# Kernel tuning notes

Measured on AMD Instinct MI355X. Metric: run time of the kernel, lower is better.

The kernel has to match this reference:

```python
import jax, jax.numpy as jnp
import numpy as np
import math

B, S, HID = 2, 2048, 1024
NH = 16
HD = HID // NH          # 64
VD = HD // 2            # 32 value dim
TD = HD - VD            # 32 type dim
EPS = 1e-6


def setup_inputs() -> dict:
    key = jax.random.key(0)
    ks = jax.random.split(key, 12)
    std = 1.0 / math.sqrt(HID)
    xav = math.sqrt(6.0 / (TD + TD))
    return {
        "x": jax.random.normal(ks[0], (B, S, HID), dtype=jnp.float32),
        "q_w": jax.random.uniform(ks[1], (HID, HID), jnp.float32, -std, std),
        "q_b": jax.random.uniform(ks[2], (HID,), jnp.float32, -std, std),
        "k_w": jax.random.uniform(ks[3], (HID, HID), jnp.float32, -std, std),
        "k_b": jax.random.uniform(ks[4], (HID,), jnp.float32, -std, std),
        "v_w": jax.random.uniform(ks[5], (HID, HID), jnp.float32, -std, std),
        "v_b": jax.random.uniform(ks[6], (HID,), jnp.float32, -std, std),
        "out_w": jax.random.uniform(ks[7], (HID, HID), jnp.float32, -std, std),
        "out_b": jax.random.uniform(ks[8], (HID,), jnp.float32, -std, std),
        "type_bilinear": jax.random.uniform(ks[9], (NH, TD, TD), jnp.float32, -xav, xav),
        "type_bias": jnp.full((NH,), 2.0, dtype=jnp.float32),
        "mask": jnp.ones((B, S), dtype=jnp.int32),
    }


def reference(x, q_w, q_b, k_w, k_b, v_w, v_b, out_w, out_b, type_bilinear, type_bias, mask):
    # projections: [B,S,HID] -> [B,NH,S,HD]
    def proj(w, b):
        y = jnp.einsum("bsi,io->bso", x, w) + b
        return y.reshape(B, S, NH, HD).transpose(0, 2, 1, 3)

    q = proj(q_w, q_b)
    k = proj(k_w, k_b)
    v = proj(v_w, v_b)

    q_val, q_type = q[..., :VD], q[..., VD:]
    k_val, k_type = k[..., :VD], k[..., VD:]

    # standard value score: [B,NH,S,S]
    val_scores = jnp.einsum("bhqd,bhkd->bhqk", q_val, k_val) / math.sqrt(VD)

    # per-head bilinear type score: q_type @ W_h @ k_type^T + bias_h
    qt = jnp.einsum("bhqd,hde->bhqe", q_type, type_bilinear)
    type_scores = jnp.einsum("bhqe,bhke->bhqk", qt, k_type) + type_bias[None, :, None, None]
    type_unif = jax.nn.sigmoid(type_scores)

    scores = val_scores + jnp.log(type_unif + EPS)

    # mask: [B,S] -> broadcast over heads and query dim (keys masked)
    m = (mask[:, None, None, :] != 0)
    scores = jnp.where(m, scores, -jnp.inf)

    attn = jax.nn.softmax(scores, axis=-1)
    out = jnp.einsum("bhqk,bhkd->bhqd", attn, v)          # [B,NH,S,HD]
    out = out.transpose(0, 2, 1, 3).reshape(B, S, HID)
    return jnp.einsum("bsi,io->bso", out, out_w) + out_b
```

## Files before the change

### kernel.cpp

```cpp
#include <hip/hip_runtime.h>
#include <hip/hip_bf16.h>
#include <math.h>

typedef __attribute__((ext_vector_type(8))) short bf16x8;
typedef __attribute__((ext_vector_type(4))) short bf16x4;
typedef __attribute__((ext_vector_type(4))) float f32x4;
typedef __attribute__((ext_vector_type(4))) int   i32x4;

#define NHh 16
#define Sq  2048
#define HIDq 1024
#define HDq 64
#define LOG2E 1.4426950408889634f

#if __has_builtin(__builtin_amdgcn_exp2f)
#define EXP2F(x) __builtin_amdgcn_exp2f(x)
#else
#define EXP2F(x) exp2f(x)
#endif
#if __has_builtin(__builtin_amdgcn_rcpf)
#define RCPF(x) __builtin_amdgcn_rcpf(x)
#else
#define RCPF(x) (1.0f/(x))
#endif

#if __has_builtin(__builtin_amdgcn_mfma_f32_16x16x16bf16_1k)
__device__ __forceinline__ f32x4 MFMA16(bf16x4 a, bf16x4 b, f32x4 c){
  return __builtin_amdgcn_mfma_f32_16x16x16bf16_1k(a, b, c, 0, 0, 0);
}
#else
__device__ __forceinline__ f32x4 MFMA16(bf16x4 a, bf16x4 b, f32x4 c){
  asm volatile("v_mfma_f32_16x16x16_bf16 %0, %1, %2, %0\n\ts_nop 7\n\ts_nop 7"
               : "+v"(c) : "v"(a), "v"(b));
  return c;
}
#endif

__device__ __forceinline__ unsigned short f2bf(float f){
  union { float f; unsigned u; } v; v.f = f;
  unsigned r = v.u + 0x7fffu + ((v.u >> 16) & 1u);
  return (unsigned short)(r >> 16);
}
__device__ __forceinline__ float bf2f(unsigned short s){
  union { unsigned u; float f; } v; v.u = ((unsigned)s) << 16;
  return v.f;
}
__device__ __forceinline__ unsigned pk2bf(float lo, float hi){
  union { __hip_bfloat162 h; unsigned u; } w;
  w.h = __float22bfloat162_rn(make_float2(lo, hi));
  return w.u;
}

__device__ __forceinline__ void gload_lds16(const unsigned short* g, unsigned short* l){
  __builtin_amdgcn_global_load_lds(
      (const __attribute__((address_space(1))) unsigned int*)g,
      (__attribute__((address_space(3))) unsigned int*)l, 16, 0, 0);
}

__global__ __launch_bounds__(256) void convert_x(const float* __restrict__ in,
                                                 unsigned short* __restrict__ out, int n8,
                                                 const int* __restrict__ mask,
                                                 unsigned short* __restrict__ Mbf){
  int bid = blockIdx.x;
  int nmain = gridDim.x - 2;
  if (bid >= nmain){
    int base = (bid - nmain)*2048 + threadIdx.x*8;
    #pragma unroll
    for (int j=0;j<8;j++) Mbf[base+j] = mask[base+j] ? (unsigned short)0x3F80 : (unsigned short)0;
    return;
  }
  int i = bid*256 + threadIdx.x;
  if (i >= n8) return;
  const f32x4* p = (const f32x4*)(in + (size_t)i*8);
  f32x4 a = p[0], b = p[1];
  union { unsigned short us[8]; i32x4 v; } o;
  #pragma unroll
  for (int j=0;j<4;j++){ o.us[j] = f2bf(a[j]); o.us[4+j] = f2bf(b[j]); }
  *(i32x4*)(out + (size_t)i*8) = o.v;
}

__global__ __launch_bounds__(256) void transpose_w(const float* __restrict__ w0, const float* __restrict__ w1,
                                                   const float* __restrict__ w2, const float* __restrict__ w3,
                                                   unsigned short* __restrict__ wT){
  __shared__ float tile[32][33];
  int z = blockIdx.z;
  const float* w = (z==0)?w0:(z==1)?w1:(z==2)?w2:w3;
  unsigned short* dst = wT + (size_t)z*HIDq*HIDq;
  int tx = threadIdx.x, ty = threadIdx.y;
  int n0 = blockIdx.x*32, k0 = blockIdx.y*32;
  #pragma unroll
  for (int i=ty;i<32;i+=8) tile[i][tx] = w[(size_t)(k0+i)*HIDq + n0+tx];
  __syncthreads();
  #pragma unroll
  for (int i=ty;i<32;i+=8) dst[(size_t)(n0+i)*HIDq + k0+tx] = f2bf(tile[tx][i]);
}

__device__ __forceinline__ void gemm_core_gl(const unsigned short* __restrict__ Ag,
                                             const unsigned short* __restrict__ Bg,
                                             unsigned short* As, unsigned short* Bs,
                                             int t, int wv, int lane, int wr, int wc, int lr, int g,
                                             f32x4 acc[4][4]){
  for (int k0=0; k0<HIDq; k0+=64){
    __syncthreads();
    #pragma unroll
    for (int j=0;j<4;j++){
      int flat = (j*4+wv)*64 + lane;
      int row = flat>>3, c = flat&7;
      int srcc = (c ^ (row&7))*8;
      gload_lds16(Ag + (size_t)row*HIDq + k0 + srcc, &As[flat*8]);
      gload_lds16(Bg + (size_t)row*HIDq + k0 + srcc, &Bs[flat*8]);
    }
    __syncthreads();
    #pragma unroll
    for (int ks=0; ks<2; ks++){
      bf16x8 af[4], bfv[4];
      #pragma unroll
      for (int m=0;m<4;m++){
        int rr = wr + m*16 + lr;
        af[m]  = *(bf16x8*)&As[rr*64 + (((ks*4+g) ^ (rr&7))*8)];
      }
      #pragma unroll
      for (int n=0;n<4;n++){
        int rr = wc + n*16 + lr;
        bfv[n] = *(bf16x8*)&Bs[rr*64 + (((ks*4+g) ^ (rr&7))*8)];
      }
      #pragma unroll
      for (int n=0;n<4;n++)
        #pragma unroll
        for (int m=0;m<4;m++)
          acc[n][m] = __builtin_amdgcn_mfma_f32_16x16x32_bf16(bfv[n], af[m], acc[n][m], 0,0,0);
    }
  }
}

__global__ __launch_bounds__(256) void gemm_qkv(const unsigned short* __restrict__ xbf,
    const unsigned short* __restrict__ wT,
    const float* __restrict__ q_b, const float* __restrict__ k_b, const float* __restrict__ v_b,
    const int* __restrict__ mask,
    unsigned short* __restrict__ Qeff, unsigned short* __restrict__ Keff,
    unsigned short* __restrict__ Vt){
  __shared__ unsigned short As[128*64];
  __shared__ unsigned short Bs[128*64];
  const int t = threadIdx.x;
  const int wv = t>>6, lane = t&63, g = lane>>4, lr = lane&15;
  const int wr = (wv>>1)*64, wc = (wv&1)*64;
  f32x4 acc[4][4] = {};
  const int xb = blockIdx.x, yb = blockIdx.y;
  const float VS = 0.25501335f;

  if (xb < 16){
    const int row0 = yb*128, col0 = xb*128;
    gemm_core_gl(xbf + (size_t)row0*HIDq, wT + (size_t)col0*HIDq, As, Bs, t, wv, lane, wr, wc, lr, g, acc);
    #pragma unroll
    for (int n=0;n<4;n++){
      #pragma unroll
      for (int m=0;m<4;m++){
        int row = row0 + wr + m*16 + lr;
        int b_ = row>>11, ss = row&2047;
        int colb = col0 + wc + n*16 + g*4;
        int seg = colb>>10, cw = colb&1023;
        int hh = cw>>6, d = cw&63;
        const float* bp = seg ? k_b : q_b;
        f32x4 bb = *(const f32x4*)&bp[cw];
        float sc = seg ? 1.0f : (d < 32 ? VS : -LOG2E);
        unsigned short* E = seg ? Keff : Qeff;
        float v0 = (acc[n][m][0]+bb[0])*sc, v1 = (acc[n][m][1]+bb[1])*sc;
        float v2 = (acc[n][m][2]+bb[2])*sc, v3 = (acc[n][m][3]+bb[3])*sc;
        union { unsigned u[2]; unsigned long long ll; } W;
        W.u[0] = pk2bf(v0,v1); W.u[1] = pk2bf(v2,v3);
        *(unsigned long long*)&E[(((size_t)b_*NHh+hh)*Sq+ss)*HDq + d] = W.ll;
      }
    }
  } else {
    const int row0 = (xb-16)*128, col0 = yb*128;
    gemm_core_gl(wT + (size_t)2*HIDq*HIDq + (size_t)row0*HIDq, xbf + (size_t)col0*HIDq,
                 As, Bs, t, wv, lane, wr, wc, lr, g, acc);
    #pragma unroll
    for (int n=0;n<4;n++){
      #pragma unroll
      for (int m=0;m<4;m++){
        int chan = row0 + wr + m*16 + lr;
        int hh = chan>>6, d = chan&63;
        float bv = v_b[chan];
        int colb = col0 + wc + n*16 + g*4;
        int b_ = colb>>11, ss = colb&2047;
        i32x4 mk = *(const i32x4*)&mask[(size_t)b_*Sq + ss];
        float m0 = mk[0]?1.f:0.f, m1 = mk[1]?1.f:0.f, m2 = mk[2]?1.f:0.f, m3 = mk[3]?1.f:0.f;
        union { unsigned u[2]; unsigned long long ll; } W;
        W.u[0] = pk2bf((acc[n][m][0]+bv)*m0, (acc[n][m][1]+bv)*m1);
        W.u[1] = pk2bf((acc[n][m][2]+bv)*m2, (acc[n][m][3]+bv)*m3);
        *(unsigned long long*)&Vt[(((size_t)b_*NHh+hh)*HDq + d)*Sq + ss] = W.ll;
      }
    }
  }
}

__global__ __launch_bounds__(256) void gemm_out(const unsigned short* __restrict__ A,
                                                const unsigned short* __restrict__ Bt,
                                                const float* __restrict__ bias,
                                                float* __restrict__ C){
  __shared__ unsigned short As[128*64];
  __shared__ unsigned short Bs[64*64];
  const int t = threadIdx.x;
  const int wv = t>>6, lane = t&63, g = lane>>4, lr = lane&15;
  const int wr = (wv>>1)*64, wc = (wv&1)*32;
  const int row0 = blockIdx.y*128, col0 = blockIdx.x*64;
  f32x4 acc[2][4] = {};
  for (int k0=0; k0<HIDq; k0+=64){
    __syncthreads();
    #pragma unroll
    for (int j=0;j<4;j++){
      int flat = t + j*256;
      int row = flat>>3, c = flat&7;
      int srcc = (c ^ (row&7))*8;
      gload_lds16(A + (size_t)(row0+row)*HIDq + k0 + srcc, &As[flat*8]);
    }
    #pragma unroll
    for (int j=0;j<2;j++){
      int flat = t + j*256;
      int row = flat>>3, c = flat&7;
      int srcc = (c ^ (row&7))*8;
      gload_lds16(Bt + (size_t)(col0+row)*HIDq + k0 + srcc, &Bs[flat*8]);
    }
    __syncthreads();
    #pragma unroll
    for (int ks=0; ks<2; ks++){
      bf16x8 af[4], bfv[2];
      #pragma unroll
      for (int m=0;m<4;m++){
        int rr = wr + m*16 + lr;
        af[m]  = *(bf16x8*)&As[rr*64 + (((ks*4+g) ^ (rr&7))*8)];
      }
      #pragma unroll
      for (int n=0;n<2;n++){
        int rr = wc + n*16 + lr;
        bfv[n] = *(bf16x8*)&Bs[rr*64 + (((ks*4+g) ^ (rr&7))*8)];
      }
      #pragma unroll
      for (int n=0;n<2;n++)
        #pragma unroll
        for (int m=0;m<4;m++)
          acc[n][m] = __builtin_amdgcn_mfma_f32_16x16x32_bf16(bfv[n], af[m], acc[n][m], 0,0,0);
    }
  }
  #pragma unroll
  for (int n=0;n<2;n++){
    #pragma unroll
    for (int m=0;m<4;m++){
      int row = row0 + wr + m*16 + lr;
      int colb = col0 + wc + n*16 + g*4;
      f32x4 bb = *(const f32x4*)&bias[colb];
      f32x4 o = acc[n][m] + bb;
      *(f32x4*)&C[(size_t)row*HIDq + colb] = o;
    }
  }
}

__global__ __launch_bounds__(256,2) void attn_kernel(
    const unsigned short* __restrict__ Qe, const unsigned short* __restrict__ Ke,
    const unsigned short* __restrict__ Vt, const float* __restrict__ Tb,
    const float* __restrict__ tbias, const unsigned short* __restrict__ Mbf,
    unsigned short* __restrict__ Obuf)
{
  __shared__ __align__(16) unsigned char smem[36864];
  unsigned short* Kb0 = (unsigned short*)smem;
  unsigned short* Kb1 = (unsigned short*)(smem + 8192);
  unsigned short* Vb0 = (unsigned short*)(smem + 16384);
  unsigned short* Vb1 = (unsigned short*)(smem + 24576);
  unsigned short* Msk = (unsigned short*)(smem + 32768);
  float* qls = (float*)smem;
  unsigned short* qtls = (unsigned short*)(smem + 24576);

  const int t = threadIdx.x;
  const int dd = blockIdx.x;
  const int slot = dd>>3, xcd = dd&7;
  const int x = slot & 15;
  const int bh = ((slot>>4)<<3) | xcd;
  const int h = bh & 15, b = bh >> 4;
  const int q0 = x*128;
  const int wv = t>>6, lane = t&63, g = lane>>4, lr = lane&15;

  const unsigned short* Qb  = Qe + (((size_t)b*NHh+h)*Sq + q0)*HDq;
  const unsigned short* Kb  = Ke + ((size_t)b*NHh+h)*(size_t)Sq*HDq;
  const unsigned short* Vtb = Vt + ((size_t)b*NHh+h)*(size_t)HDq*Sq;
  const unsigned short* Mbfb = Mbf + (size_t)b*Sq;

  {
    int row = t>>1, c8 = (t&1)*16;
    bf16x8 v0 = *(const bf16x8*)(Qb + (size_t)row*HDq + 32 + c8);
    bf16x8 v1 = *(const bf16x8*)(Qb + (size_t)row*HDq + 32 + c8 + 8);
    #pragma unroll
    for (int j=0;j<8;j++){
      qls[row*33 + c8 + j]     = bf2f((unsigned short)v0[j]);
      qls[row*33 + c8 + 8 + j] = bf2f((unsigned short)v1[j]);
    }
  }
  __syncthreads();
  {
    const float* Th = Tb + (size_t)h*1024;
    #pragma unroll
    for (int rp=0; rp<2; rp++){
      int row = rp*64 + (t&63), e0 = (t>>6)*8;
      float a[8] = {};
      #pragma unroll 4
      for (int d=0; d<32; d++){
        float qd = qls[row*33 + d];
        const f32x4* tp = (const f32x4*)(Th + d*32 + e0);
        f32x4 t0 = tp[0], t1 = tp[1];
        a[0]+=qd*t0[0]; a[1]+=qd*t0[1]; a[2]+=qd*t0[2]; a[3]+=qd*t0[3];
        a[4]+=qd*t1[0]; a[5]+=qd*t1[1]; a[6]+=qd*t1[2]; a[7]+=qd*t1[3];
      }
      union { unsigned u[2]; unsigned long long ll; } W0, W1;
      W0.u[0]=pk2bf(a[0],a[1]); W0.u[1]=pk2bf(a[2],a[3]);
      W1.u[0]=pk2bf(a[4],a[5]); W1.u[1]=pk2bf(a[6],a[7]);
      *(unsigned long long*)&qtls[row*40 + e0]     = W0.ll;
      *(unsigned long long*)&qtls[row*40 + e0 + 4] = W1.ll;
    }
  }
  bf16x8 qvf0 = *(const bf16x8*)(Qb + (size_t)(wv*32+lr)*HDq + g*8);
  bf16x8 qvf1 = *(const bf16x8*)(Qb + (size_t)(wv*32+16+lr)*HDq + g*8);
  __syncthreads();
  bf16x8 qtn0 = *(const bf16x8*)&qtls[(wv*32+lr)*40 + g*8];
  bf16x8 qtn1 = *(const bf16x8*)&qtls[(wv*32+16+lr)*40 + g*8];
  __syncthreads();

  gload_lds16(Mbfb + t*8, Msk + t*8);
  #pragma unroll
  for (int i=0;i<2;i++){
    int c = t + i*256;
    int kr = c>>3, kc = c&7;
    gload_lds16(Kb + (size_t)kr*HDq + ((kc ^ (kr&7))*8), Kb0 + c*8);
    int vd = c>>3, vc = c&7;
    gload_lds16(Vtb + (size_t)vd*Sq + ((vc ^ (vd&7))*8), Vb0 + c*8);
  }
  __syncthreads();

  const float tbn = -tbias[h]*LOG2E;
  const f32x4 tbc = {tbn,tbn,tbn,tbn};
  const f32x4 zf = {0.f,0.f,0.f,0.f};
  f32x4 oT0[4] = {}, oT1[4] = {};
  f32x4 lsum0 = {0.f,0.f,0.f,0.f}, lsum1 = {0.f,0.f,0.f,0.f};

  auto phase = [&](const unsigned short* Kc, const unsigned short* Vc, int key0,
                   bool doStage, int keyN, unsigned short* Kn, unsigned short* Vn){
    if (doStage){
      #pragma unroll
      for (int i=0;i<2;i++){
        int c = t + i*256;
        int kr = c>>3, kc = c&7;
        gload_lds16(Kb + (size_t)(keyN+kr)*HDq + ((kc ^ (kr&7))*8), Kn + c*8);
        int vd = c>>3, vc = c&7;
        gload_lds16(Vtb + (size_t)vd*Sq + keyN + ((vc ^ (vd&7))*8), Vn + c*8);
      }
      asm volatile("s_waitcnt vmcnt(4)" ::: "memory");
    } else {
      asm volatile("s_waitcnt vmcnt(0)" ::: "memory");
    }
    __builtin_amdgcn_sched_barrier(0);
    __builtin_amdgcn_s_barrier();

    f32x4 sv0[4], st0[4], sv1[4], st1[4];
    __builtin_amdgcn_s_setprio(1);
    #pragma unroll
    for (int ks=0; ks<4; ks++){
      const unsigned short* kb = Kc + (ks*16+lr)*64;
      bf16x8 kf0 = *(const bf16x8*)(kb + (((g  ) ^ (lr&7))*8));
      bf16x8 kf1 = *(const bf16x8*)(kb + (((4+g) ^ (lr&7))*8));
      sv0[ks] = __builtin_amdgcn_mfma_f32_16x16x32_bf16(kf0, qvf0, zf, 0,0,0);
      st0[ks] = __builtin_amdgcn_mfma_f32_16x16x32_bf16(kf1, qtn0, tbc, 0,0,0);
      sv1[ks] = __builtin_amdgcn_mfma_f32_16x16x32_bf16(kf0, qvf1, zf, 0,0,0);
      st1[ks] = __builtin_amdgcn_mfma_f32_16x16x32_bf16(kf1, qtn1, tbc, 0,0,0);
    }
    __builtin_amdgcn_s_setprio(0);
    bf16x4 pa0[4], pa1[4];
    #pragma unroll
    for (int ks=0; ks<4; ks++){
      {
        float p0 = EXP2F(sv0[ks][0]) * RCPF(1.f + EXP2F(st0[ks][0]));
        float p1 = EXP2F(sv0[ks][1]) * RCPF(1.f + EXP2F(st0[ks][1]));
        float p2 = EXP2F(sv0[ks][2]) * RCPF(1.f + EXP2F(st0[ks][2]));
        float p3 = EXP2F(sv0[ks][3]) * RCPF(1.f + EXP2F(st0[ks][3]));
        union { unsigned u[2]; bf16x4 v; } P_;
        P_.u[0] = pk2bf(p0,p1); P_.u[1] = pk2bf(p2,p3);
        pa0[ks] = P_.v;
      }
      {
        float p0 = EXP2F(sv1[ks][0]) * RCPF(1.f + EXP2F(st1[ks][0]));
        float p1 = EXP2F(sv1[ks][1]) * RCPF(1.f + EXP2F(st1[ks][1]));
        float p2 = EXP2F(sv1[ks][2]) * RCPF(1.f + EXP2F(st1[ks][2]));
        float p3 = EXP2F(sv1[ks][3]) * RCPF(1.f + EXP2F(st1[ks][3]));
        union { unsigned u[2]; bf16x4 v; } P_;
        P_.u[0] = pk2bf(p0,p1); P_.u[1] = pk2bf(p2,p3);
        pa1[ks] = P_.v;
      }
    }
    #pragma unroll
    for (int ks=0; ks<4; ks++){
      bf16x4 mfr = *(const bf16x4*)(Msk + key0 + ks*16 + g*4);
      __builtin_amdgcn_s_setprio(1);
      lsum0 = MFMA16(pa0[ks], mfr, lsum0);
      lsum1 = MFMA16(pa1[ks], mfr, lsum1);
      #pragma unroll
      for (int db=0; db<4; db++){
        bf16x4 vf = *(const bf16x4*)(Vc + (db*16+lr)*64 + (((2*ks + (g>>1)) ^ (lr&7))*8 + 4*(g&1)));
        oT0[db] = MFMA16(pa0[ks], vf, oT0[db]);
        oT1[db] = MFMA16(pa1[ks], vf, oT1[db]);
      }
      __builtin_amdgcn_s_setprio(0);
    }
    __builtin_amdgcn_s_barrier();
  };

  for (int kt=0; kt<Sq; kt+=128){
    phase(Kb0, Vb0, kt,      true,           kt+64,  Kb1, Vb1);
    phase(Kb1, Vb1, kt+64,   kt+128 < Sq,    kt+128, Kb0, Vb0);
  }

  float linv0[4], linv1[4];
  #pragma unroll
  for (int r=0;r<4;r++){
    linv0[r] = (lsum0[r] > 0.f) ? RCPF(lsum0[r]) : 0.f;
    linv1[r] = (lsum1[r] > 0.f) ? RCPF(lsum1[r]) : 0.f;
  }
  {
    unsigned short* Ob = Obuf + ((size_t)b*Sq + (q0 + wv*32 + g*4))*HIDq + h*HDq + lr;
    #pragma unroll
    for (int db=0; db<4; db++)
      #pragma unroll
      for (int r=0;r<4;r++)
        Ob[(size_t)r*HIDq + db*16] = f2bf(oT0[db][r]*linv0[r]);
  }
  {
    unsigned short* Ob = Obuf + ((size_t)b*Sq + (q0 + wv*32 + 16 + g*4))*HIDq + h*HDq + lr;
    #pragma unroll
    for (int db=0; db<4; db++)
      #pragma unroll
      for (int r=0;r<4;r++)
        Ob[(size_t)r*HIDq + db*16] = f2bf(oT1[db][r]*linv1[r]);
  }
}

extern "C" void kernel_launch(void* const* d_in, const int* in_sizes, int n_in,
                              void* d_out, int out_size, void* d_ws, size_t ws_size,
                              hipStream_t stream) {
  const float* x     = (const float*)d_in[0];
  const float* q_w   = (const float*)d_in[1];
  const float* q_b   = (const float*)d_in[2];
  const float* k_w   = (const float*)d_in[3];
  const float* k_b   = (const float*)d_in[4];
  const float* v_w   = (const float*)d_in[5];
  const float* v_b   = (const float*)d_in[6];
  const float* out_w = (const float*)d_in[7];
  const float* out_b = (const float*)d_in[8];
  const float* Tb    = (const float*)d_in[9];
  const float* tbias = (const float*)d_in[10];
  const int*   mask  = (const int*)d_in[11];

  const size_t MROWS = 4096;
  unsigned short* xbf  = (unsigned short*)d_ws;
  unsigned short* wT   = xbf  + MROWS*HIDq;
  unsigned short* Qeff = wT   + (size_t)4*HIDq*HIDq;
  unsigned short* Keff = Qeff + MROWS*HIDq;
  unsigned short* Vt   = Keff + MROWS*HIDq;
  unsigned short* Obuf = Vt   + MROWS*HIDq;
  unsigned short* Mbf  = Obuf + MROWS*HIDq;

  int n8 = (int)(MROWS*HIDq/8);
  convert_x<<<dim3(n8/256 + 2), dim3(256), 0, stream>>>(x, xbf, n8, mask, Mbf);
  transpose_w<<<dim3(32,32,4), dim3(32,8), 0, stream>>>(q_w, k_w, v_w, out_w, wT);

  gemm_qkv<<<dim3(24,32), dim3(256), 0, stream>>>(xbf, wT, q_b, k_b, v_b, mask, Qeff, Keff, Vt);

  attn_kernel<<<dim3(512), dim3(256), 0, stream>>>(Qeff, Keff, Vt, Tb, tbias, Mbf, Obuf);

  gemm_out<<<dim3(16,32), dim3(256), 0, stream>>>(Obuf, wT + (size_t)3*HIDq*HIDq, out_b, (float*)d_out);
}
```

Baseline: 154.3 us.

## Split attention over key halves, fold type bilinear into Q weights

The attention kernel now splits the key range into two halves, doubling the grid to 1024 blocks with a higher occupancy target. Each half writes a normalized partial output and its row sums, and a new merge kernel combines them. The per-block type-bilinear transform of Q is removed; a fold_T kernel multiplies the Q weights and bias by the bilinear matrix once per call, so the QKV GEMM emits the transformed Q directly. The convert and transpose prep kernels are fused into one launch, and gemm_qkv blocks are remapped across XCDs. The cost is an extra merge pass, partial results stored in bf16, and buffer reuse of the xbf and wT regions for partials.

```diff
diff --git a/kernel.cpp b/kernel.cpp
--- a/kernel.cpp
+++ b/kernel.cpp
@@ -57,42 +57,80 @@
       (__attribute__((address_space(3))) unsigned int*)l, 16, 0, 0);
 }
 
-__global__ __launch_bounds__(256) void convert_x(const float* __restrict__ in,
-                                                 unsigned short* __restrict__ out, int n8,
-                                                 const int* __restrict__ mask,
-                                                 unsigned short* __restrict__ Mbf){
+__global__ __launch_bounds__(256) void prep(const float* __restrict__ x,
+                                            unsigned short* __restrict__ xbf,
+                                            const int* __restrict__ mask,
+                                            unsigned short* __restrict__ Mbf,
+                                            const float* __restrict__ w0, const float* __restrict__ w1,
+                                            const float* __restrict__ w2, const float* __restrict__ w3,
+                                            unsigned short* __restrict__ wT){
   int bid = blockIdx.x;
-  int nmain = gridDim.x - 2;
-  if (bid >= nmain){
-    int base = (bid - nmain)*2048 + threadIdx.x*8;
+  int t = threadIdx.x;
+  if (bid < 2048){
+    int i = bid*256 + t;
+    const f32x4* p = (const f32x4*)(x + (size_t)i*8);
+    f32x4 a = p[0], b = p[1];
+    union { unsigned short us[8]; i32x4 v; } o;
+    #pragma unroll
+    for (int j=0;j<4;j++){ o.us[j] = f2bf(a[j]); o.us[4+j] = f2bf(b[j]); }
+    *(i32x4*)(xbf + (size_t)i*8) = o.v;
+  } else if (bid < 2050){
+    int base = (bid - 2048)*2048 + t*8;
     #pragma unroll
     for (int j=0;j<8;j++) Mbf[base+j] = mask[base+j] ? (unsigned short)0x3F80 : (unsigned short)0;
-    return;
-  }
-  int i = bid*256 + threadIdx.x;
-  if (i >= n8) return;
-  const f32x4* p = (const f32x4*)(in + (size_t)i*8);
-  f32x4 a = p[0], b = p[1];
-  union { unsigned short us[8]; i32x4 v; } o;
-  #pragma unroll
-  for (int j=0;j<4;j++){ o.us[j] = f2bf(a[j]); o.us[4+j] = f2bf(b[j]); }
-  *(i32x4*)(out + (size_t)i*8) = o.v;
-}
-
-__global__ __launch_bounds__(256) void transpose_w(const float* __restrict__ w0, const float* __restrict__ w1,
-                                                   const float* __restrict__ w2, const float* __restrict__ w3,
-                                                   unsigned short* __restrict__ wT){
-  __shared__ float tile[32][33];
-  int z = blockIdx.z;
-  const float* w = (z==0)?w0:(z==1)?w1:(z==2)?w2:w3;
-  unsigned short* dst = wT + (size_t)z*HIDq*HIDq;
-  int tx = threadIdx.x, ty = threadIdx.y;
-  int n0 = blockIdx.x*32, k0 = blockIdx.y*32;
-  #pragma unroll
-  for (int i=ty;i<32;i+=8) tile[i][tx] = w[(size_t)(k0+i)*HIDq + n0+tx];
+  } else {
+    __shared__ float tile[32][33];
+    int bid2 = bid - 2050;
+    int z = bid2 >> 10, rem = bid2 & 1023;
+    int bx = rem & 31, by = rem >> 5;
+    const float* w = (z==0)?w0:(z==1)?w1:(z==2)?w2:w3;
+    unsigned short* dst = wT + (size_t)z*HIDq*HIDq;
+    int tx = t & 31, ty = t >> 5;
+    int n0 = bx*32, k0 = by*32;
+    #pragma unroll
+    for (int i=ty;i<32;i+=8) tile[i][tx] = w[(size_t)(k0+i)*HIDq + n0+tx];
+    __syncthreads();
+    #pragma unroll
+    for (int i=ty;i<32;i+=8) dst[(size_t)(n0+i)*HIDq + k0+tx] = f2bf(tile[tx][i]);
+  }
+}
+
+__global__ __launch_bounds__(256) void fold_T(const float* __restrict__ q_w,
+                                              const float* __restrict__ q_b,
+                                              const float* __restrict__ Tb,
+                                              unsigned short* __restrict__ wTq,
+                                              float* __restrict__ qb_eff){
+  __shared__ float Ts[32][33];
+  const int h = blockIdx.x;
+  const int t = threadIdx.x;
+  if (t < 128){
+    int d = t>>2, e0 = (t&3)*8;
+    #pragma unroll
+    for (int j=0;j<8;j++) Ts[d][e0+j] = Tb[h*1024 + d*32 + e0 + j];
+  }
   __syncthreads();
-  #pragma unroll
-  for (int i=ty;i<32;i+=8) dst[(size_t)(n0+i)*HIDq + k0+tx] = f2bf(tile[tx][i]);
+  const int col0 = h*64 + 32;
+  if (t < 32){
+    float a = 0.f;
+    #pragma unroll 8
+    for (int d=0; d<32; d++) a += q_b[col0+d]*Ts[d][t];
+    qb_eff[col0 + t] = a;
+  } else if (t < 64){
+    qb_eff[h*64 + (t-32)] = q_b[h*64 + (t-32)];
+  }
+  for (int k = t; k < HIDq; k += 256){
+    float qr[32];
+    const float* src = q_w + (size_t)k*HIDq + col0;
+    #pragma unroll 8
+    for (int d=0;d<32;d++) qr[d] = src[d];
+    #pragma unroll 4
+    for (int e=0;e<32;e++){
+      float a = 0.f;
+      #pragma unroll 8
+      for (int d=0;d<32;d++) a += qr[d]*Ts[d][e];
+      wTq[(size_t)(col0+e)*HIDq + k] = f2bf(a);
+    }
+  }
 }
 
 __device__ __forceinline__ void gemm_core_gl(const unsigned short* __restrict__ Ag,
@@ -135,7 +173,7 @@
 
 __global__ __launch_bounds__(256) void gemm_qkv(const unsigned short* __restrict__ xbf,
     const unsigned short* __restrict__ wT,
-    const float* __restrict__ q_b, const float* __restrict__ k_b, const float* __restrict__ v_b,
+    const float* __restrict__ qb_eff, const float* __restrict__ k_b, const float* __restrict__ v_b,
     const int* __restrict__ mask,
     unsigned short* __restrict__ Qeff, unsigned short* __restrict__ Keff,
     unsigned short* __restrict__ Vt){
@@ -145,7 +183,10 @@
   const int wv = t>>6, lane = t&63, g = lane>>4, lr = lane&15;
   const int wr = (wv>>1)*64, wc = (wv&1)*64;
   f32x4 acc[4][4] = {};
-  const int xb = blockIdx.x, yb = blockIdx.y;
+  const int bid = blockIdx.x;
+  const int xcd = bid & 7, idx = bid >> 3;
+  const int xb = (idx % 3)*8 + xcd;
+  const int yb = idx / 3;
   const float VS = 0.25501335f;
 
   if (xb < 16){
@@ -160,7 +201,7 @@
         int colb = col0 + wc + n*16 + g*4;
         int seg = colb>>10, cw = colb&1023;
         int hh = cw>>6, d = cw&63;
-        const float* bp = seg ? k_b : q_b;
+        const float* bp = seg ? k_b : qb_eff;
         f32x4 bb = *(const f32x4*)&bp[cw];
         float sc = seg ? 1.0f : (d < 32 ? VS : -LOG2E);
         unsigned short* E = seg ? Keff : Qeff;
@@ -256,75 +297,41 @@
   }
 }
 
-__global__ __launch_bounds__(256,2) void attn_kernel(
+__global__ __launch_bounds__(256,4) void attn_kernel(
     const unsigned short* __restrict__ Qe, const unsigned short* __restrict__ Ke,
-    const unsigned short* __restrict__ Vt, const float* __restrict__ Tb,
+    const unsigned short* __restrict__ Vt,
     const float* __restrict__ tbias, const unsigned short* __restrict__ Mbf,
-    unsigned short* __restrict__ Obuf)
+    unsigned short* __restrict__ Obuf, unsigned short* __restrict__ pOB,
+    float* __restrict__ pLA, float* __restrict__ pLB)
 {
-  __shared__ __align__(16) unsigned char smem[36864];
+  __shared__ __align__(16) unsigned char smem[34816];
   unsigned short* Kb0 = (unsigned short*)smem;
   unsigned short* Kb1 = (unsigned short*)(smem + 8192);
   unsigned short* Vb0 = (unsigned short*)(smem + 16384);
   unsigned short* Vb1 = (unsigned short*)(smem + 24576);
   unsigned short* Msk = (unsigned short*)(smem + 32768);
-  float* qls = (float*)smem;
-  unsigned short* qtls = (unsigned short*)(smem + 24576);
 
   const int t = threadIdx.x;
   const int dd = blockIdx.x;
   const int slot = dd>>3, xcd = dd&7;
   const int x = slot & 15;
-  const int bh = ((slot>>4)<<3) | xcd;
+  const int sh = (slot>>4) & 1;
+  const int bh = ((slot>>5)<<3) | xcd;
   const int h = bh & 15, b = bh >> 4;
   const int q0 = x*128;
   const int wv = t>>6, lane = t&63, g = lane>>4, lr = lane&15;
 
   const unsigned short* Qb  = Qe + (((size_t)b*NHh+h)*Sq + q0)*HDq;
-  const unsigned short* Kb  = Ke + ((size_t)b*NHh+h)*(size_t)Sq*HDq;
-  const unsigned short* Vtb = Vt + ((size_t)b*NHh+h)*(size_t)HDq*Sq;
-  const unsigned short* Mbfb = Mbf + (size_t)b*Sq;
-
-  {
-    int row = t>>1, c8 = (t&1)*16;
-    bf16x8 v0 = *(const bf16x8*)(Qb + (size_t)row*HDq + 32 + c8);
-    bf16x8 v1 = *(const bf16x8*)(Qb + (size_t)row*HDq + 32 + c8 + 8);
-    #pragma unroll
-    for (int j=0;j<8;j++){
-      qls[row*33 + c8 + j]     = bf2f((unsigned short)v0[j]);
-      qls[row*33 + c8 + 8 + j] = bf2f((unsigned short)v1[j]);
-    }
-  }
-  __syncthreads();
-  {
-    const float* Th = Tb + (size_t)h*1024;
-    #pragma unroll
-    for (int rp=0; rp<2; rp++){
-      int row = rp*64 + (t&63), e0 = (t>>6)*8;
-      float a[8] = {};
-      #pragma unroll 4
-      for (int d=0; d<32; d++){
-        float qd = qls[row*33 + d];
-        const f32x4* tp = (const f32x4*)(Th + d*32 + e0);
-        f32x4 t0 = tp[0], t1 = tp[1];
-        a[0]+=qd*t0[0]; a[1]+=qd*t0[1]; a[2]+=qd*t0[2]; a[3]+=qd*t0[3];
-        a[4]+=qd*t1[0]; a[5]+=qd*t1[1]; a[6]+=qd*t1[2]; a[7]+=qd*t1[3];
-      }
-      union { unsigned u[2]; unsigned long long ll; } W0, W1;
-      W0.u[0]=pk2bf(a[0],a[1]); W0.u[1]=pk2bf(a[2],a[3]);
-      W1.u[0]=pk2bf(a[4],a[5]); W1.u[1]=pk2bf(a[6],a[7]);
-      *(unsigned long long*)&qtls[row*40 + e0]     = W0.ll;
-      *(unsigned long long*)&qtls[row*40 + e0 + 4] = W1.ll;
-    }
-  }
+  const unsigned short* Kb  = Ke + ((size_t)b*NHh+h)*(size_t)Sq*HDq + (size_t)sh*1024*HDq;
+  const unsigned short* Vtb = Vt + ((size_t)b*NHh+h)*(size_t)HDq*Sq + sh*1024;
+  const unsigned short* Mbfb = Mbf + (size_t)b*Sq + sh*1024;
+
   bf16x8 qvf0 = *(const bf16x8*)(Qb + (size_t)(wv*32+lr)*HDq + g*8);
+  bf16x8 qtn0 = *(const bf16x8*)(Qb + (size_t)(wv*32+lr)*HDq + 32 + g*8);
   bf16x8 qvf1 = *(const bf16x8*)(Qb + (size_t)(wv*32+16+lr)*HDq + g*8);
-  __syncthreads();
-  bf16x8 qtn0 = *(const bf16x8*)&qtls[(wv*32+lr)*40 + g*8];
-  bf16x8 qtn1 = *(const bf16x8*)&qtls[(wv*32+16+lr)*40 + g*8];
-  __syncthreads();
-
-  gload_lds16(Mbfb + t*8, Msk + t*8);
+  bf16x8 qtn1 = *(const bf16x8*)(Qb + (size_t)(wv*32+16+lr)*HDq + 32 + g*8);
+
+  if (wv < 2) gload_lds16(Mbfb + (wv*64+lane)*8, Msk + (wv*64+lane)*8);
   #pragma unroll
   for (int i=0;i<2;i++){
     int c = t + i*256;
@@ -411,9 +418,9 @@
     __builtin_amdgcn_s_barrier();
   };
 
-  for (int kt=0; kt<Sq; kt+=128){
-    phase(Kb0, Vb0, kt,      true,           kt+64,  Kb1, Vb1);
-    phase(Kb1, Vb1, kt+64,   kt+128 < Sq,    kt+128, Kb0, Vb0);
+  for (int lk=0; lk<1024; lk+=128){
+    phase(Kb0, Vb0, lk,      true,            lk+64,  Kb1, Vb1);
+    phase(Kb1, Vb1, lk+64,   lk+128 < 1024,   lk+128, Kb0, Vb0);
   }
 
   float linv0[4], linv1[4];
@@ -422,22 +429,62 @@
     linv0[r] = (lsum0[r] > 0.f) ? RCPF(lsum0[r]) : 0.f;
     linv1[r] = (lsum1[r] > 0.f) ? RCPF(lsum1[r]) : 0.f;
   }
-  {
-    unsigned short* Ob = Obuf + ((size_t)b*Sq + (q0 + wv*32 + g*4))*HIDq + h*HDq + lr;
-    #pragma unroll
-    for (int db=0; db<4; db++)
-      #pragma unroll
-      for (int r=0;r<4;r++)
-        Ob[(size_t)r*HIDq + db*16] = f2bf(oT0[db][r]*linv0[r]);
-  }
-  {
-    unsigned short* Ob = Obuf + ((size_t)b*Sq + (q0 + wv*32 + 16 + g*4))*HIDq + h*HDq + lr;
-    #pragma unroll
-    for (int db=0; db<4; db++)
-      #pragma unroll
-      for (int r=0;r<4;r++)
-        Ob[(size_t)r*HIDq + db*16] = f2bf(oT1[db][r]*linv1[r]);
-  }
+  const int pidx = bh*16 + x;
+  float* pL = sh ? pLB : pLA;
+  if (lr == 0){
+    #pragma unroll
+    for (int r=0;r<4;r++){
+      pL[pidx*128 + wv*32 + g*4 + r]      = lsum0[r];
+      pL[pidx*128 + wv*32 + 16 + g*4 + r] = lsum1[r];
+    }
+  }
+  if (sh == 0){
+    unsigned short* Ob0 = Obuf + ((size_t)b*Sq + (q0 + wv*32 + g*4))*HIDq + h*HDq + lr;
+    unsigned short* Ob1 = Obuf + ((size_t)b*Sq + (q0 + wv*32 + 16 + g*4))*HIDq + h*HDq + lr;
+    #pragma unroll
+    for (int db=0; db<4; db++){
+      #pragma unroll
+      for (int r=0;r<4;r++){
+        Ob0[(size_t)r*HIDq + db*16] = f2bf(oT0[db][r]*linv0[r]);
+        Ob1[(size_t)r*HIDq + db*16] = f2bf(oT1[db][r]*linv1[r]);
+      }
+    }
+  } else {
+    unsigned short* Pb0 = pOB + ((size_t)pidx*128 + wv*32 + g*4)*64 + lr;
+    unsigned short* Pb1 = Pb0 + 16*64;
+    #pragma unroll
+    for (int db=0; db<4; db++){
+      #pragma unroll
+      for (int r=0;r<4;r++){
+        Pb0[(size_t)r*64 + db*16] = f2bf(oT0[db][r]*linv0[r]);
+        Pb1[(size_t)r*64 + db*16] = f2bf(oT1[db][r]*linv1[r]);
+      }
+    }
+  }
+}
+
+__global__ __launch_bounds__(256) void merge_halves(unsigned short* __restrict__ Obuf,
+                                                    const unsigned short* __restrict__ pOB,
+                                                    const float* __restrict__ pLA,
+                                                    const float* __restrict__ pLB){
+  int gid = blockIdx.x*256 + threadIdx.x;
+  int d8 = gid & 7;
+  int q  = (gid>>3) & 127;
+  int idx = gid >> 10;
+  float lA = pLA[idx*128 + q], lB = pLB[idx*128 + q];
+  float ls = lA + lB;
+  float inv = (ls > 0.f) ? RCPF(ls) : 0.f;
+  float wA = lA*inv, wB = lB*inv;
+  int bh = idx>>4, x = idx&15;
+  int b = bh>>4, h = bh&15;
+  size_t oaddr = ((size_t)b*Sq + (x*128 + q))*HIDq + h*HDq + d8*8;
+  bf16x8 a = *(const bf16x8*)(Obuf + oaddr);
+  bf16x8 c = *(const bf16x8*)(pOB + ((size_t)idx*128 + q)*64 + d8*8);
+  union { unsigned short us[8]; i32x4 v; } o;
+  #pragma unroll
+  for (int j=0;j<8;j++)
+    o.us[j] = f2bf(bf2f((unsigned short)a[j])*wA + bf2f((unsigned short)c[j])*wB);
+  *(i32x4*)(Obuf + oaddr) = o.v;
 }
 
 extern "C" void kernel_launch(void* const* d_in, const int* in_sizes, int n_in,
@@ -464,14 +511,18 @@
   unsigned short* Vt   = Keff + MROWS*HIDq;
   unsigned short* Obuf = Vt   + MROWS*HIDq;
   unsigned short* Mbf  = Obuf + MROWS*HIDq;
-
-  int n8 = (int)(MROWS*HIDq/8);
-  convert_x<<<dim3(n8/256 + 2), dim3(256), 0, stream>>>(x, xbf, n8, mask, Mbf);
-  transpose_w<<<dim3(32,32,4), dim3(32,8), 0, stream>>>(q_w, k_w, v_w, out_w, wT);
-
-  gemm_qkv<<<dim3(24,32), dim3(256), 0, stream>>>(xbf, wT, q_b, k_b, v_b, mask, Qeff, Keff, Vt);
-
-  attn_kernel<<<dim3(512), dim3(256), 0, stream>>>(Qeff, Keff, Vt, Tb, tbias, Mbf, Obuf);
+  float*          qb_eff = (float*)(Mbf + 4096);
+  unsigned short* pOB = xbf;
+  float* pLA = (float*)wT;
+  float* pLB = pLA + 65536;
+
+  prep<<<dim3(6146), dim3(256), 0, stream>>>(x, xbf, mask, Mbf, q_w, k_w, v_w, out_w, wT);
+  fold_T<<<dim3(16), dim3(256), 0, stream>>>(q_w, q_b, Tb, wT, qb_eff);
+
+  gemm_qkv<<<dim3(768), dim3(256), 0, stream>>>(xbf, wT, qb_eff, k_b, v_b, mask, Qeff, Keff, Vt);
+
+  attn_kernel<<<dim3(1024), dim3(256), 0, stream>>>(Qeff, Keff, Vt, tbias, Mbf, Obuf, pOB, pLA, pLB);
+  merge_halves<<<dim3(2048), dim3(256), 0, stream>>>(Obuf, pOB, pLA, pLB);
 
   gemm_out<<<dim3(16,32), dim3(256), 0, stream>>>(Obuf, wT + (size_t)3*HIDq*HIDq, out_b, (float*)d_out);
 }
```

Result: slower. 273.2 us (+77.0%).
